# Kernel optimization log

Hardware: AMD Instinct MI355X
Metric: run time of the kernel (lower is better)

The kernel has to match this reference:

```python
import jax, jax.numpy as jnp
import numpy as np
from jax import lax

N, E = 50000, 800000
IN_DIM = 128
HID = 128
HEADS = 8
DPH = HID // HEADS
RH = 128
BETA = 0.1
GAMMA = 1.0
SVI_ITERS = 5
NUM_LAYERS = 2


def seg_lse(z, seg, n):
    # segment-wise logsumexp along axis 0; z: [E] or [E,H]
    m = jax.ops.segment_max(z, seg, num_segments=n)
    m0 = jnp.where(jnp.isfinite(m), m, 0.0)
    s = jax.ops.segment_sum(jnp.exp(z - m0[seg]), seg, num_segments=n)
    return jnp.where(s > 0, jnp.log(jnp.maximum(s, 1e-38)) + m0, -jnp.inf)


def seg_softmax(e, seg, n):
    lse = seg_lse(e, seg, n)
    return jnp.exp(e - lse[seg])


def gat_layer(h_in, W, a_src, a_dst, src, dst, n):
    h = (h_in @ W).reshape(n, HEADS, DPH)                       # [N,H,D]
    al_s = jnp.einsum('nhd,hd->nh', h, a_src)                   # [N,H]
    al_d = jnp.einsum('nhd,hd->nh', h, a_dst)
    e = jax.nn.leaky_relu(al_s[src] + al_d[dst], 0.2)           # [E,H]
    attn = seg_softmax(e, dst, n)                               # softmax over incoming edges
    out = jax.ops.segment_sum(attn[:, :, None] * h[src], dst, num_segments=n)
    return out.reshape(n, HEADS * DPH), attn.mean(-1)           # [N,HID], [E]


def mlp2(z, W1, b1, w2, b2):
    return jax.nn.relu(z @ W1 + b1) @ w2 + b2                   # [E]


def svi_hop(r, src, dst, n, has_out):
    # soft value iteration: V[s] = beta*logsumexp_e(Q_e/beta), Q_e = r_e + gamma*V[dst]
    def body(V, _):
        Q = r + GAMMA * V[dst]
        V2 = jnp.where(has_out, BETA * seg_lse(Q / BETA, src, n), 0.0)
        return V2, None
    V, _ = lax.scan(body, jnp.zeros(n, r.dtype), None, length=SVI_ITERS)
    Q = r + GAMMA * V[dst]
    logz = seg_lse(Q / BETA, src, n)
    log_pi = Q / BETA - logz[src]                               # per-edge log pi*(a|s=src)
    return Q, log_pi


def setup_inputs() -> dict:
    key = jax.random.key(0)
    ks = jax.random.split(key, 20)
    s = 0.05
    inp = {
        'x': jax.random.normal(ks[0], (N, IN_DIM), jnp.float32),
        'edge_index': jax.random.randint(ks[1], (2, E), 0, N, jnp.int64),
        'W0': jax.random.normal(ks[2], (IN_DIM, HID), jnp.float32) * s,
        'as0': jax.random.normal(ks[3], (HEADS, DPH), jnp.float32) * s,
        'ad0': jax.random.normal(ks[4], (HEADS, DPH), jnp.float32) * s,
        'W1': jax.random.normal(ks[5], (HID, HID), jnp.float32) * s,
        'as1': jax.random.normal(ks[6], (HEADS, DPH), jnp.float32) * s,
        'ad1': jax.random.normal(ks[7], (HEADS, DPH), jnp.float32) * s,
        'Ws1': jax.random.normal(ks[8], (4, RH), jnp.float32) * s,
        'bs1': jnp.zeros((RH,), jnp.float32),
        'ws2': jax.random.normal(ks[9], (RH,), jnp.float32) * s,
        'bs2': jnp.zeros((), jnp.float32),
        'Wm1': jax.random.normal(ks[10], (2 * HID, RH), jnp.float32) * s,
        'bm1': jnp.zeros((RH,), jnp.float32),
        'wm2': jax.random.normal(ks[11], (RH,), jnp.float32) * s,
        'bm2': jnp.zeros((), jnp.float32),
        'lam1': jnp.ones((), jnp.float32),
    }
    return inp


def reference(x, edge_index, W0, as0, ad0, W1, as1, ad1,
              Ws1, bs1, ws2, bs2, Wm1, bm1, wm2, bm2, lam1):
    n = x.shape[0]
    src, dst = edge_index[0], edge_index[1]

    # --- GAT encoder trajectory: hidden_per_hop = [x, h1], attn_per_hop = [a1, a2]
    h1, a1 = gat_layer(x, W0, as0, ad0, src, dst, n)
    h1 = jax.nn.elu(h1)
    h2, a2 = gat_layer(h1, W1, as1, ad1, src, dst, n)
    hidden = [x, h1]
    attn = [a1, a2]

    # --- structural per-edge features (degrees)
    ones_e = jnp.ones(src.shape[0], x.dtype)
    deg_out = jax.ops.segment_sum(ones_e, src, num_segments=n)
    deg_in = jax.ops.segment_sum(ones_e, dst, num_segments=n)
    sf = jnp.stack([deg_out[src], deg_in[dst],
                    jnp.log1p(deg_out[src]), jnp.log1p(deg_in[dst])], axis=-1)  # [E,4]
    r_str = mlp2(sf, Ws1, bs1, ws2, bs2)

    has_out = deg_out > 0

    # --- per-hop rewards: r = r_str + lambda1 * r_sem  (use_tmp=False)
    rewards = []
    for t in range(NUM_LAYERS):
        h = hidden[t]
        r_sem = mlp2(jnp.concatenate([h[src], h[dst]], axis=-1), Wm1, bm1, wm2, bm2)
        rewards.append(r_str + lam1 * r_sem)

    # --- soft value iteration per hop
    log_pi_star = [svi_hop(r, src, dst, n, has_out)[1] for r in rewards]

    # --- observed policy from attention (renormalized over outgoing edges)
    log_pi_obs = []
    for a in attn:
        la = jnp.log(a + 1e-12)
        log_pi_obs.append(la - seg_lse(la, src, n)[src])

    # --- NLL loss: sum_t scatter_add(-p_obs * log_pi*) over src, mean over nodes
    per_src_nll = jnp.zeros(n, x.dtype)
    for t in range(NUM_LAYERS):
        p = jnp.exp(log_pi_obs[t])
        per_src_nll = per_src_nll + jax.ops.segment_sum(-p * log_pi_star[t], src, num_segments=n)
    loss = per_src_nll.mean()

    # --- KL(pi_obs || pi*) anomaly score per node
    score = jnp.zeros(n, x.dtype)
    for t in range(NUM_LAYERS):
        p = jnp.exp(log_pi_obs[t])
        score = score + jax.ops.segment_sum(p * (log_pi_obs[t] - log_pi_star[t]), src, num_segments=n)

    return loss, score
```

## Files before the change

kernel.cpp:

```cpp
#include <hip/hip_runtime.h>
#include <math.h>

#define NN 50000
#define NE 800000
#define BETAF 0.1f
#define INVB 10.0f

typedef _Float16 half8v __attribute__((ext_vector_type(8)));
typedef _Float16 half2v __attribute__((ext_vector_type(2)));
typedef float floatx4 __attribute__((ext_vector_type(4)));

__device__ __forceinline__ float sc_(float s, float m, float mn){
  return (s == 0.f) ? 0.f : s * expf(m - mn);
}
__device__ __forceinline__ void red16(float& v){
  v += __shfl_xor(v, 1, 64); v += __shfl_xor(v, 2, 64);
  v += __shfl_xor(v, 4, 64); v += __shfl_xor(v, 8, 64);
}
__device__ __forceinline__ void lse16(float& m, float& s){
  #pragma unroll
  for (int off = 1; off < 16; off <<= 1){
    float mo = __shfl_xor(m, off, 64), so = __shfl_xor(s, off, 64);
    float mn = fmaxf(m, mo);
    s = sc_(s, m, mn) + sc_(so, mo, mn); m = mn;
  }
}
__device__ __forceinline__ float dot2acc(half2v a, half2v b, float c){
#if __has_builtin(__builtin_amdgcn_fdot2)
  return __builtin_amdgcn_fdot2(a, b, c, false);
#else
  return c + (float)a[0]*(float)b[0] + (float)a[1]*(float)b[1];
#endif
}

__launch_bounds__(256)
__global__ void k_hist(const int* __restrict__ ei, int* __restrict__ cs, int* __restrict__ cd){
  int e = blockIdx.x*256 + threadIdx.x;
  if (e >= NE) return;
  atomicAdd(&cs[ei[e]], 1);
  atomicAdd(&cd[ei[NE + e]], 1);
}

__launch_bounds__(256)
__global__ void k_scan_a(const int* __restrict__ inA, const int* __restrict__ inB,
                         int* __restrict__ outA, int* __restrict__ outB,
                         int* __restrict__ partA, int* __restrict__ partB, int n){
  const int* in = blockIdx.y ? inB : inA;
  int* out = blockIdx.y ? outB : outA;
  int* part = blockIdx.y ? partB : partA;
  int i = blockIdx.x*256 + threadIdx.x;
  int v = (i < n) ? in[i] : 0;
  int lane = threadIdx.x & 63, wid = threadIdx.x >> 6;
  int x = v;
  #pragma unroll
  for (int off = 1; off < 64; off <<= 1){
    int t = __shfl_up(x, off, 64);
    if (lane >= off) x += t;
  }
  __shared__ int wsum[4];
  if (lane == 63) wsum[wid] = x;
  __syncthreads();
  int base = 0;
  #pragma unroll
  for (int w = 0; w < 4; ++w) if (w < wid) base += wsum[w];
  if (i < n) out[i] = base + x - v;
  if (threadIdx.x == 255) part[blockIdx.x] = base + x;
}

__launch_bounds__(256)
__global__ void k_scan_b(int* __restrict__ partA, int* __restrict__ partB, int np){
  int* part = blockIdx.y ? partB : partA;
  int i = threadIdx.x;
  int v = (i < np) ? part[i] : 0;
  int lane = threadIdx.x & 63, wid = threadIdx.x >> 6;
  int x = v;
  #pragma unroll
  for (int off = 1; off < 64; off <<= 1){
    int t = __shfl_up(x, off, 64);
    if (lane >= off) x += t;
  }
  __shared__ int wsum[4];
  if (lane == 63) wsum[wid] = x;
  __syncthreads();
  int base = 0;
  #pragma unroll
  for (int w = 0; w < 4; ++w) if (w < wid) base += wsum[w];
  if (i < np) part[i] = base + x - v;
}

__launch_bounds__(256)
__global__ void k_scan_c(int* __restrict__ outA, int* __restrict__ outB,
                         int* __restrict__ curA, int* __restrict__ curB,
                         const int* __restrict__ partA, const int* __restrict__ partB, int n){
  int* out = blockIdx.y ? outB : outA;
  int* cur = blockIdx.y ? curB : curA;
  const int* part = blockIdx.y ? partB : partA;
  int i = blockIdx.x*256 + threadIdx.x;
  if (i < n){
    int f = out[i] + part[blockIdx.x];
    out[i] = f;
    cur[i] = f;
  }
  if (blockIdx.x == 0 && threadIdx.x == 0) out[n] = NE;
}

__launch_bounds__(256)
__global__ void k_scatter(const int* __restrict__ ei, int* __restrict__ cur_s, int* __restrict__ cur_d,
                          int* __restrict__ src_of_j, int* __restrict__ dst_csr,
                          int* __restrict__ src_dord, int* __restrict__ rs_dord){
  int e = blockIdx.x*256 + threadIdx.x;
  if (e >= NE) return;
  int s = ei[e], d = ei[NE + e];
  int js = atomicAdd(&cur_s[s], 1);
  src_of_j[js] = s;
  dst_csr[js] = d;
  int jd = atomicAdd(&cur_d[d], 1);
  src_dord[jd] = s;
  rs_dord[jd] = js;
}

__launch_bounds__(256)
__global__ void k_deg(const int* __restrict__ row_s, const int* __restrict__ row_d,
                      unsigned char* __restrict__ d8o, unsigned char* __restrict__ d8i){
  int n = blockIdx.x*256 + threadIdx.x;
  if (n >= NN) return;
  int a = row_s[n+1] - row_s[n];
  int b = row_d[n+1] - row_d[n];
  d8o[n] = (unsigned char)(a > 127 ? 127 : a);
  d8i[n] = (unsigned char)(b > 127 ? 127 : b);
}

__launch_bounds__(256)
__global__ void k_prepw(const float* __restrict__ W0, const float* __restrict__ W1,
                        const float* __restrict__ Wm1, _Float16* __restrict__ Wt){
  int idx = blockIdx.x*256 + threadIdx.x;
  if (idx >= 4*128*128) return;
  int mat = idx >> 14, rem = idx & 16383;
  int n = rem >> 7, k = rem & 127;
  const float* src = (mat == 0) ? W0 : (mat == 1) ? W1 : (mat == 2) ? Wm1 : (Wm1 + 128*128);
  Wt[idx] = (_Float16)src[k*128 + n];
}

__launch_bounds__(256)
__global__ void k_strtab(const float* __restrict__ Ws1, const float* __restrict__ bs1,
                         const float* __restrict__ ws2, const float* __restrict__ bs2,
                         float* __restrict__ tab){
  int idx = blockIdx.x*256 + threadIdx.x;
  if (idx >= 128*128) return;
  float du = (float)(idx >> 7), di = (float)(idx & 127);
  float lo = log1pf(du), li = log1pf(di);
  float acc = 0.f;
  for (int c = 0; c < 128; ++c){
    float z = du*Ws1[c] + di*Ws1[128+c] + lo*Ws1[256+c] + li*Ws1[384+c] + bs1[c];
    acc += fmaxf(z, 0.f)*ws2[c];
  }
  tab[idx] = acc + bs2[0];
}

template<int AF16, int SECOND>
__launch_bounds__(256)
__global__ void k_gemm3(const void* __restrict__ Ap,
                        const _Float16* __restrict__ Bt0, const _Float16* __restrict__ Bt1,
                        const _Float16* __restrict__ Bt2,
                        const float* __restrict__ bm1,
                        const float* __restrict__ a_s, const float* __restrict__ a_d,
                        _Float16* __restrict__ Hout, _Float16* __restrict__ U01,
                        _Float16* __restrict__ V01,
                        float* __restrict__ alS, float* __restrict__ alD, int M){
  int wv = threadIdx.x >> 6, lane = threadIdx.x & 63;
  int m = lane & 15, q = lane >> 4;
  int row = blockIdx.x*64 + wv*16 + m;
  int arow = (row < M) ? row : (M-1);
  half8v af[4];
  if (AF16){
    const half8v* Ar = (const half8v*)((const _Float16*)Ap + (size_t)arow*128);
    #pragma unroll
    for (int kt = 0; kt < 4; ++kt) af[kt] = Ar[kt*4 + q];
  } else {
    const float* Ar = (const float*)Ap + (size_t)arow*128;
    #pragma unroll
    for (int kt = 0; kt < 4; ++kt){
      const float4* f = (const float4*)(Ar + kt*32 + q*8);
      float4 a0 = f[0], a1 = f[1];
      half8v h;
      h[0]=(_Float16)a0.x; h[1]=(_Float16)a0.y; h[2]=(_Float16)a0.z; h[3]=(_Float16)a0.w;
      h[4]=(_Float16)a1.x; h[5]=(_Float16)a1.y; h[6]=(_Float16)a1.z; h[7]=(_Float16)a1.w;
      af[kt] = h;
    }
  }
  floatx4 acc0[8], acc1[8], acc2[8];
  #pragma unroll
  for (int ct = 0; ct < 8; ++ct){
    #pragma unroll
    for (int r = 0; r < 4; ++r){ acc0[ct][r]=0.f; acc1[ct][r]=0.f; acc2[ct][r]=0.f; }
  }
  #pragma unroll
  for (int ct = 0; ct < 8; ++ct){
    const half8v* Br0 = (const half8v*)(Bt0 + (size_t)(ct*16 + m)*128);
    const half8v* Br1 = (const half8v*)(Bt1 + (size_t)(ct*16 + m)*128);
    const half8v* Br2 = (const half8v*)(Bt2 + (size_t)(ct*16 + m)*128);
    #pragma unroll
    for (int kt = 0; kt < 4; ++kt){
      acc0[ct] = __builtin_amdgcn_mfma_f32_16x16x32_f16(af[kt], Br0[kt*4 + q], acc0[ct], 0, 0, 0);
      acc1[ct] = __builtin_amdgcn_mfma_f32_16x16x32_f16(af[kt], Br1[kt*4 + q], acc1[ct], 0, 0, 0);
      acc2[ct] = __builtin_amdgcn_mfma_f32_16x16x32_f16(af[kt], Br2[kt*4 + q], acc2[ct], 0, 0, 0);
    }
  }
  int rb = blockIdx.x*64 + wv*16 + q*4;
  #pragma unroll
  for (int ct = 0; ct < 8; ++ct){
    float cs = a_s[ct*16 + m], cd = a_d[ct*16 + m];
    #pragma unroll
    for (int r = 0; r < 4; ++r){
      float ps = acc0[ct][r]*cs, pd = acc0[ct][r]*cd;
      #pragma unroll
      for (int off = 1; off < 16; off <<= 1){
        ps += __shfl_xor(ps, off, 64);
        pd += __shfl_xor(pd, off, 64);
      }
      int rr = rb + r;
      if (m == 0 && rr < M){ alS[rr*8 + ct] = ps; alD[rr*8 + ct] = pd; }
    }
  }
  #pragma unroll
  for (int ct = 0; ct < 8; ++ct){
    int col = ct*16 + m;
    float bv = bm1[col];
    #pragma unroll
    for (int r = 0; r < 4; ++r){
      int rr = rb + r;
      if (rr < M){
        if (SECOND == 0) Hout[(size_t)rr*128 + col] = (_Float16)acc0[ct][r];
        U01[(size_t)rr*256 + SECOND*128 + col] = (_Float16)(acc1[ct][r] + bv);
        V01[(size_t)rr*256 + SECOND*128 + col] = (_Float16)acc2[ct][r];
      }
    }
  }
}

template<bool AGG>
__launch_bounds__(256)
__global__ void k_att(const int* __restrict__ row_d, const int* __restrict__ src_dord,
                      const int* __restrict__ rs_dord,
                      const float* __restrict__ alS, const float* __restrict__ alD,
                      const _Float16* __restrict__ H,
                      float* __restrict__ a_csr, _Float16* __restrict__ h1){
  __shared__ float zbuf[4][64*8];
  int wv = threadIdx.x >> 6;
  int node = blockIdx.x*4 + wv;
  if (node >= NN) return;
  int lane = threadIdx.x & 63;
  int j0 = row_d[node], j1 = row_d[node+1];
  int deg = j1 - j0;
  if (deg == 0){
    if (AGG){
      half2v z; z[0] = (_Float16)0; z[1] = (_Float16)0;
      ((half2v*)(h1 + (size_t)node*128))[lane] = z;
    }
    return;
  }
  int head = lane & 7, slot = lane >> 3;
  float ad = alD[node*8 + head];
  float m = -INFINITY, ssum = 0.f;

  if (deg <= 64){
    for (int e = slot; e < deg; e += 8){
      int s = src_dord[j0 + e];
      float z = alS[s*8 + head] + ad;
      z = (z >= 0.f) ? z : 0.2f*z;
      zbuf[wv][e*8 + head] = z;
      float mn = fmaxf(m, z);
      ssum = sc_(ssum, m, mn) + expf(z - mn);
      m = mn;
    }
    #pragma unroll
    for (int off = 8; off < 64; off <<= 1){
      float mo = __shfl_xor(m, off, 64);
      float so = __shfl_xor(ssum, off, 64);
      float mn = fmaxf(m, mo);
      ssum = sc_(ssum, m, mn) + sc_(so, mo, mn);
      m = mn;
    }
    float inv_s = 1.f / ssum;
    for (int e = slot; e < deg; e += 8){
      float a = expf(zbuf[wv][e*8 + head] - m) * inv_s;
      zbuf[wv][e*8 + head] = a;
      float asum = a;
      asum += __shfl_xor(asum, 1, 64);
      asum += __shfl_xor(asum, 2, 64);
      asum += __shfl_xor(asum, 4, 64);
      if (head == 0) a_csr[rs_dord[j0 + e]] = asum * 0.125f;
    }
    if (AGG){
      __asm__ volatile("s_waitcnt lgkmcnt(0)" ::: "memory");
      int h2 = lane >> 3;
      float ax = 0.f, ay = 0.f;
      const half2v* Hv = (const half2v*)H;
      for (int e = 0; e < deg; ++e){
        int s = src_dord[j0 + e];
        float a = zbuf[wv][e*8 + h2];
        half2v hv = Hv[(size_t)s*64 + lane];
        ax += a*(float)hv[0];
        ay += a*(float)hv[1];
      }
      ax = (ax > 0.f) ? ax : expm1f(ax);
      ay = (ay > 0.f) ? ay : expm1f(ay);
      half2v o; o[0] = (_Float16)ax; o[1] = (_Float16)ay;
      ((half2v*)(h1 + (size_t)node*128))[lane] = o;
    }
  } else {
    for (int j = j0 + slot; j < j1; j += 8){
      int s = src_dord[j];
      float z = alS[s*8 + head] + ad;
      z = (z >= 0.f) ? z : 0.2f*z;
      float mn = fmaxf(m, z);
      ssum = sc_(ssum, m, mn) + expf(z - mn);
      m = mn;
    }
    #pragma unroll
    for (int off = 8; off < 64; off <<= 1){
      float mo = __shfl_xor(m, off, 64);
      float so = __shfl_xor(ssum, off, 64);
      float mn = fmaxf(m, mo);
      ssum = sc_(ssum, m, mn) + sc_(so, mo, mn);
      m = mn;
    }
    float inv_s = 1.f / ssum;
    for (int j = j0 + slot; j < j1; j += 8){
      int s = src_dord[j];
      float z = alS[s*8 + head] + ad;
      z = (z >= 0.f) ? z : 0.2f*z;
      float a = expf(z - m) * inv_s;
      float asum = a;
      asum += __shfl_xor(asum, 1, 64);
      asum += __shfl_xor(asum, 2, 64);
      asum += __shfl_xor(asum, 4, 64);
      if (head == 0) a_csr[rs_dord[j]] = asum * 0.125f;
    }
    if (AGG){
      int h2 = lane >> 3;
      float m2 = __shfl(m, h2*8, 64);
      float is2 = __shfl(inv_s, h2*8, 64);
      float ad2 = alD[node*8 + h2];
      float ax = 0.f, ay = 0.f;
      const half2v* Hv = (const half2v*)H;
      for (int j = j0; j < j1; ++j){
        int s = src_dord[j];
        float z = alS[s*8 + h2] + ad2;
        z = (z >= 0.f) ? z : 0.2f*z;
        float a = expf(z - m2) * is2;
        half2v hv = Hv[(size_t)s*64 + lane];
        ax += a*(float)hv[0];
        ay += a*(float)hv[1];
      }
      ax = (ax > 0.f) ? ax : expm1f(ax);
      ay = (ay > 0.f) ? ay : expm1f(ay);
      half2v o; o[0] = (_Float16)ax; o[1] = (_Float16)ay;
      ((half2v*)(h1 + (size_t)node*128))[lane] = o;
    }
  }
}

__launch_bounds__(256)
__global__ void k_edge5(const int* __restrict__ src_of_j, const int* __restrict__ dst_csr,
                        const unsigned char* __restrict__ d8o, const unsigned char* __restrict__ d8i,
                        const float* __restrict__ tab,
                        const _Float16* __restrict__ U01, const _Float16* __restrict__ V01,
                        const float* __restrict__ wm2, const float* __restrict__ bm2,
                        const float* __restrict__ lam1,
                        float* __restrict__ rcsr0, float* __restrict__ rcsr1){
  __shared__ _Float16 wml[128];
  if (threadIdx.x < 128) wml[threadIdx.x] = (_Float16)wm2[threadIdx.x];
  __syncthreads();
  int j = blockIdx.x*16 + (threadIdx.x >> 4);
  if (j >= NE) return;
  int t = threadIdx.x & 15;
  int s = src_of_j[j], d = dst_csr[j];
  const half8v* ur = (const half8v*)(U01 + (size_t)s*256);
  const half8v* vr = (const half8v*)(V01 + (size_t)d*256);
  half8v a = ur[t] + vr[t];
  half8v b = ur[16 + t] + vr[16 + t];
  #pragma unroll
  for (int k = 0; k < 8; ++k){
    a[k] = (a[k] > (_Float16)0) ? a[k] : (_Float16)0;
    b[k] = (b[k] > (_Float16)0) ? b[k] : (_Float16)0;
  }
  const half8v* wl = (const half8v*)wml;
  half8v w = wl[t];
  float r0 = 0.f, r1 = 0.f;
  #pragma unroll
  for (int c = 0; c < 4; ++c){
    half2v aa = {a[2*c], a[2*c+1]};
    half2v bb = {b[2*c], b[2*c+1]};
    half2v ww = {w[2*c], w[2*c+1]};
    r0 = dot2acc(aa, ww, r0);
    r1 = dot2acc(bb, ww, r1);
  }
  red16(r0); red16(r1);
  if (t == 0){
    float rstr = tab[((int)d8o[s] << 7) | (int)d8i[d]];
    float lam = lam1[0], bb2 = bm2[0];
    rcsr0[j] = rstr + lam*(r0 + bb2);
    rcsr1[j] = rstr + lam*(r1 + bb2);
  }
}

__launch_bounds__(256)
__global__ void k_svi(const int* __restrict__ row_s, const int* __restrict__ dst_csr,
                      const float* __restrict__ r0, const float* __restrict__ r1,
                      const float* __restrict__ V0in, const float* __restrict__ V1in,
                      float* __restrict__ out0, float* __restrict__ out1){
  int node = blockIdx.x*16 + (threadIdx.x >> 4);
  if (node >= NN) return;
  int t = threadIdx.x & 15;
  int j0 = row_s[node], j1 = row_s[node+1];
  if (j0 == j1){
    if (t == 0){ out0[node] = 0.f; out1[node] = 0.f; }
    return;
  }
  float m0 = -INFINITY, s0 = 0.f, m1 = -INFINITY, s1 = 0.f;
  for (int j = j0 + t; j < j1; j += 16){
    int d = dst_csr[j];
    float q0 = (r0[j] + V0in[d]) * INVB;
    float q1 = (r1[j] + V1in[d]) * INVB;
    float mn0 = fmaxf(m0, q0);
    s0 = sc_(s0, m0, mn0) + expf(q0 - mn0); m0 = mn0;
    float mn1 = fmaxf(m1, q1);
    s1 = sc_(s1, m1, mn1) + expf(q1 - mn1); m1 = mn1;
  }
  lse16(m0, s0); lse16(m1, s1);
  if (t == 0){
    out0[node] = BETAF*(logf(s0) + m0);
    out1[node] = BETAF*(logf(s1) + m1);
  }
}

__launch_bounds__(256)
__global__ void k_final2(const int* __restrict__ row_s, const int* __restrict__ dst_csr,
                         const float* __restrict__ a0, const float* __restrict__ a1,
                         const float* __restrict__ r0, const float* __restrict__ r1,
                         const float* __restrict__ V0, const float* __restrict__ V1,
                         float* __restrict__ out, float* __restrict__ partial){
  int node = blockIdx.x*16 + (threadIdx.x >> 4);
  int t = threadIdx.x & 15;
  float nll = 0.f;
  if (node < NN){
    int j0 = row_s[node], j1 = row_s[node+1];
    if (j0 == j1){
      if (t == 0) out[1 + node] = 0.f;
    } else {
      float mq0=-INFINITY, sq0=0.f, mq1=-INFINITY, sq1=0.f;
      float ma0=-INFINITY, sa0=0.f, ma1=-INFINITY, sa1=0.f;
      for (int j = j0 + t; j < j1; j += 16){
        int d = dst_csr[j];
        float q0 = (r0[j] + V0[d]) * INVB;
        float q1 = (r1[j] + V1[d]) * INVB;
        float la0 = logf(a0[j] + 1e-12f);
        float la1 = logf(a1[j] + 1e-12f);
        float mn;
        mn = fmaxf(mq0, q0); sq0 = sc_(sq0, mq0, mn) + expf(q0 - mn); mq0 = mn;
        mn = fmaxf(mq1, q1); sq1 = sc_(sq1, mq1, mn) + expf(q1 - mn); mq1 = mn;
        mn = fmaxf(ma0, la0); sa0 = sc_(sa0, ma0, mn) + expf(la0 - mn); ma0 = mn;
        mn = fmaxf(ma1, la1); sa1 = sc_(sa1, ma1, mn) + expf(la1 - mn); ma1 = mn;
      }
      lse16(mq0, sq0); lse16(mq1, sq1); lse16(ma0, sa0); lse16(ma1, sa1);
      float L0 = logf(sq0) + mq0, L1 = logf(sq1) + mq1;
      float O0 = logf(sa0) + ma0, O1 = logf(sa1) + ma1;
      float sca = 0.f;
      for (int j = j0 + t; j < j1; j += 16){
        int d = dst_csr[j];
        float la0 = logf(a0[j] + 1e-12f);
        float lp0 = la0 - O0;
        float p0 = expf(lp0);
        float ls0 = (r0[j] + V0[d]) * INVB - L0;
        nll -= p0 * ls0;
        sca += p0 * (lp0 - ls0);
        float la1 = logf(a1[j] + 1e-12f);
        float lp1 = la1 - O1;
        float p1 = expf(lp1);
        float ls1 = (r1[j] + V1[d]) * INVB - L1;
        nll -= p1 * ls1;
        sca += p1 * (lp1 - ls1);
      }
      red16(sca);
      if (t == 0) out[1 + node] = sca;
    }
  }
  #pragma unroll
  for (int off = 1; off < 64; off <<= 1) nll += __shfl_xor(nll, off, 64);
  __shared__ float wsum[4];
  if ((threadIdx.x & 63) == 0) wsum[threadIdx.x >> 6] = nll;
  __syncthreads();
  if (threadIdx.x == 0) partial[blockIdx.x] = wsum[0]+wsum[1]+wsum[2]+wsum[3];
}

__launch_bounds__(256)
__global__ void k_nllred(const float* __restrict__ partial, int np, float* __restrict__ out){
  float s = 0.f;
  for (int i = threadIdx.x; i < np; i += 256) s += partial[i];
  #pragma unroll
  for (int off = 1; off < 64; off <<= 1) s += __shfl_xor(s, off, 64);
  __shared__ float wsum[4];
  if ((threadIdx.x & 63) == 0) wsum[threadIdx.x >> 6] = s;
  __syncthreads();
  if (threadIdx.x == 0) out[0] = (wsum[0]+wsum[1]+wsum[2]+wsum[3]) * (1.f/NN);
}

extern "C" void kernel_launch(void* const* d_in, const int* in_sizes, int n_in,
                              void* d_out, int out_size, void* d_ws, size_t ws_size,
                              hipStream_t stream){
  const float* x    = (const float*)d_in[0];
  const int*   ei   = (const int*)d_in[1];
  const float* W0   = (const float*)d_in[2];
  const float* as0  = (const float*)d_in[3];
  const float* ad0  = (const float*)d_in[4];
  const float* W1   = (const float*)d_in[5];
  const float* as1  = (const float*)d_in[6];
  const float* ad1  = (const float*)d_in[7];
  const float* Ws1  = (const float*)d_in[8];
  const float* bs1  = (const float*)d_in[9];
  const float* ws2  = (const float*)d_in[10];
  const float* bs2  = (const float*)d_in[11];
  const float* Wm1  = (const float*)d_in[12];
  const float* bm1  = (const float*)d_in[13];
  const float* wm2  = (const float*)d_in[14];
  const float* bm2  = (const float*)d_in[15];
  const float* lam1 = (const float*)d_in[16];
  float* out = (float*)d_out;

  char* p = (char*)d_ws;
  auto alloc = [&](size_t bytes)->void*{
    void* r = (void*)p;
    p += (bytes + 255) & ~(size_t)255;
    return r;
  };
  _Float16* Hh   = (_Float16*)alloc((size_t)NN*128*2);
  _Float16* h1f  = (_Float16*)alloc((size_t)NN*128*2);
  _Float16* U01  = (_Float16*)alloc((size_t)NN*256*2);
  _Float16* V01  = (_Float16*)alloc((size_t)NN*256*2);
  _Float16* Wt   = (_Float16*)alloc((size_t)4*128*128*2);
  float* tab     = (float*)alloc((size_t)128*128*4);
  int*   src_of_j= (int*)alloc((size_t)NE*4);
  int*   dst_csr = (int*)alloc((size_t)NE*4);
  int*   src_dord= (int*)alloc((size_t)NE*4);
  int*   rs_dord = (int*)alloc((size_t)NE*4);
  int*   row_s   = (int*)alloc((size_t)(NN+1)*4);
  int*   row_d   = (int*)alloc((size_t)(NN+1)*4);
  int*   cur_s   = (int*)alloc((size_t)NN*4);
  int*   cur_d   = (int*)alloc((size_t)NN*4);
  int*   partA   = (int*)alloc(256*4);
  int*   partB   = (int*)alloc(256*4);
  unsigned char* d8o = (unsigned char*)alloc(NN);
  unsigned char* d8i = (unsigned char*)alloc(NN);
  float* alS     = (float*)alloc((size_t)NN*8*4);
  float* alD     = (float*)alloc((size_t)NN*8*4);
  float* acsr0   = (float*)alloc((size_t)NE*4);
  float* acsr1   = (float*)alloc((size_t)NE*4);
  float* rcsr0   = (float*)alloc((size_t)NE*4);
  float* rcsr1   = (float*)alloc((size_t)NE*4);
  float* V0a = (float*)alloc((size_t)NN*4);
  float* V0b = (float*)alloc((size_t)NN*4);
  float* V1a = (float*)alloc((size_t)NN*4);
  float* V1b = (float*)alloc((size_t)NN*4);
  float* nllpart = (float*)alloc((size_t)4*((NN+15)/16 + 1));

  _Float16* W0t = Wt;
  _Float16* W1t = Wt + 128*128;
  _Float16* Wut = Wt + 2*128*128;
  _Float16* Wvt = Wt + 3*128*128;

  const int G_E    = (NE + 255)/256;
  const int G_gemm = (NN + 63)/64;
  const int G_n4   = (NN + 3)/4;
  const int G_n16  = (NN + 15)/16;
  const int G_e16  = (NE + 15)/16;
  const int NPART  = (NN + 255)/256;

  hipMemsetAsync(cur_s, 0, (size_t)NN*4, stream);
  hipMemsetAsync(cur_d, 0, (size_t)NN*4, stream);
  k_hist<<<G_E, 256, 0, stream>>>(ei, cur_s, cur_d);
  k_scan_a<<<dim3(NPART,2), 256, 0, stream>>>(cur_s, cur_d, row_s, row_d, partA, partB, NN);
  k_scan_b<<<dim3(1,2), 256, 0, stream>>>(partA, partB, NPART);
  k_scan_c<<<dim3(NPART,2), 256, 0, stream>>>(row_s, row_d, cur_s, cur_d, partA, partB, NN);
  k_scatter<<<G_E, 256, 0, stream>>>(ei, cur_s, cur_d, src_of_j, dst_csr, src_dord, rs_dord);
  k_deg<<<(NN+255)/256, 256, 0, stream>>>(row_s, row_d, d8o, d8i);

  k_prepw<<<(4*128*128+255)/256, 256, 0, stream>>>(W0, W1, Wm1, Wt);
  k_strtab<<<(128*128+255)/256, 256, 0, stream>>>(Ws1, bs1, ws2, bs2, tab);

  k_gemm3<0,0><<<G_gemm, 256, 0, stream>>>(x, W0t, Wut, Wvt, bm1, as0, ad0,
                                           Hh, U01, V01, alS, alD, NN);
  k_att<true><<<G_n4, 256, 0, stream>>>(row_d, src_dord, rs_dord, alS, alD, Hh, acsr0, h1f);

  k_gemm3<1,1><<<G_gemm, 256, 0, stream>>>(h1f, W1t, Wut, Wvt, bm1, as1, ad1,
                                           nullptr, U01, V01, alS, alD, NN);
  k_att<false><<<G_n4, 256, 0, stream>>>(row_d, src_dord, rs_dord, alS, alD, nullptr, acsr1, nullptr);

  k_edge5<<<G_e16, 256, 0, stream>>>(src_of_j, dst_csr, d8o, d8i, tab,
                                     U01, V01, wm2, bm2, lam1, rcsr0, rcsr1);

  hipMemsetAsync(V0a, 0, (size_t)NN*4, stream);
  hipMemsetAsync(V1a, 0, (size_t)NN*4, stream);
  float* v0i = V0a; float* v0o = V0b;
  float* v1i = V1a; float* v1o = V1b;
  for (int it = 0; it < 5; ++it){
    k_svi<<<G_n16, 256, 0, stream>>>(row_s, dst_csr, rcsr0, rcsr1, v0i, v1i, v0o, v1o);
    float* t;
    t = v0i; v0i = v0o; v0o = t;
    t = v1i; v1i = v1o; v1o = t;
  }

  k_final2<<<G_n16, 256, 0, stream>>>(row_s, dst_csr, acsr0, acsr1, rcsr0, rcsr1,
                                      v0i, v1i, out, nllpart);
  k_nllred<<<1, 256, 0, stream>>>(nllpart, G_n16, out);
}
```

Measured before the change: 710.0 us.

## Pack edge index arrays, fuse SVI iterations cooperatively, precompute log attention

```diff
diff --git a/kernel.cpp b/kernel.cpp
--- a/kernel.cpp
+++ b/kernel.cpp
@@ -1,10 +1,11 @@
 #include <hip/hip_runtime.h>
+#include <hip/hip_cooperative_groups.h>
 #include <math.h>
+
+namespace cg = cooperative_groups;
 
 #define NN 50000
 #define NE 800000
-#define BETAF 0.1f
-#define INVB 10.0f
 
 typedef _Float16 half8v __attribute__((ext_vector_type(8)));
 typedef _Float16 half2v __attribute__((ext_vector_type(2)));
@@ -106,17 +107,14 @@
 
 __launch_bounds__(256)
 __global__ void k_scatter(const int* __restrict__ ei, int* __restrict__ cur_s, int* __restrict__ cur_d,
-                          int* __restrict__ src_of_j, int* __restrict__ dst_csr,
-                          int* __restrict__ src_dord, int* __restrict__ rs_dord){
+                          int2* __restrict__ sd_csr, int2* __restrict__ sr_dord){
   int e = blockIdx.x*256 + threadIdx.x;
   if (e >= NE) return;
   int s = ei[e], d = ei[NE + e];
   int js = atomicAdd(&cur_s[s], 1);
-  src_of_j[js] = s;
-  dst_csr[js] = d;
+  sd_csr[js] = make_int2(s, d);
   int jd = atomicAdd(&cur_d[d], 1);
-  src_dord[jd] = s;
-  rs_dord[jd] = js;
+  sr_dord[jd] = make_int2(s, js);
 }
 
 __launch_bounds__(256)
@@ -240,11 +238,10 @@
 
 template<bool AGG>
 __launch_bounds__(256)
-__global__ void k_att(const int* __restrict__ row_d, const int* __restrict__ src_dord,
-                      const int* __restrict__ rs_dord,
+__global__ void k_att(const int* __restrict__ row_d, const int2* __restrict__ sr_dord,
                       const float* __restrict__ alS, const float* __restrict__ alD,
                       const _Float16* __restrict__ H,
-                      float* __restrict__ a_csr, _Float16* __restrict__ h1){
+                      float* __restrict__ la_csr, _Float16* __restrict__ h1){
   __shared__ float zbuf[4][64*8];
   int wv = threadIdx.x >> 6;
   int node = blockIdx.x*4 + wv;
@@ -265,7 +262,7 @@
 
   if (deg <= 64){
     for (int e = slot; e < deg; e += 8){
-      int s = src_dord[j0 + e];
+      int s = sr_dord[j0 + e].x;
       float z = alS[s*8 + head] + ad;
       z = (z >= 0.f) ? z : 0.2f*z;
       zbuf[wv][e*8 + head] = z;
@@ -289,7 +286,7 @@
       asum += __shfl_xor(asum, 1, 64);
       asum += __shfl_xor(asum, 2, 64);
       asum += __shfl_xor(asum, 4, 64);
-      if (head == 0) a_csr[rs_dord[j0 + e]] = asum * 0.125f;
+      if (head == 0) la_csr[sr_dord[j0 + e].y] = logf(asum*0.125f + 1e-12f);
     }
     if (AGG){
       __asm__ volatile("s_waitcnt lgkmcnt(0)" ::: "memory");
@@ -297,7 +294,7 @@
       float ax = 0.f, ay = 0.f;
       const half2v* Hv = (const half2v*)H;
       for (int e = 0; e < deg; ++e){
-        int s = src_dord[j0 + e];
+        int s = sr_dord[j0 + e].x;
         float a = zbuf[wv][e*8 + h2];
         half2v hv = Hv[(size_t)s*64 + lane];
         ax += a*(float)hv[0];
@@ -310,7 +307,7 @@
     }
   } else {
     for (int j = j0 + slot; j < j1; j += 8){
-      int s = src_dord[j];
+      int s = sr_dord[j].x;
       float z = alS[s*8 + head] + ad;
       z = (z >= 0.f) ? z : 0.2f*z;
       float mn = fmaxf(m, z);
@@ -327,7 +324,7 @@
     }
     float inv_s = 1.f / ssum;
     for (int j = j0 + slot; j < j1; j += 8){
-      int s = src_dord[j];
+      int s = sr_dord[j].x;
       float z = alS[s*8 + head] + ad;
       z = (z >= 0.f) ? z : 0.2f*z;
       float a = expf(z - m) * inv_s;
@@ -335,7 +332,7 @@
       asum += __shfl_xor(asum, 1, 64);
       asum += __shfl_xor(asum, 2, 64);
       asum += __shfl_xor(asum, 4, 64);
-      if (head == 0) a_csr[rs_dord[j]] = asum * 0.125f;
+      if (head == 0) la_csr[sr_dord[j].y] = logf(asum*0.125f + 1e-12f);
     }
     if (AGG){
       int h2 = lane >> 3;
@@ -345,7 +342,7 @@
       float ax = 0.f, ay = 0.f;
       const half2v* Hv = (const half2v*)H;
       for (int j = j0; j < j1; ++j){
-        int s = src_dord[j];
+        int s = sr_dord[j].x;
         float z = alS[s*8 + h2] + ad2;
         z = (z >= 0.f) ? z : 0.2f*z;
         float a = expf(z - m2) * is2;
@@ -362,7 +359,7 @@
 }
 
 __launch_bounds__(256)
-__global__ void k_edge5(const int* __restrict__ src_of_j, const int* __restrict__ dst_csr,
+__global__ void k_edge5(const int2* __restrict__ sd,
                         const unsigned char* __restrict__ d8o, const unsigned char* __restrict__ d8i,
                         const float* __restrict__ tab,
                         const _Float16* __restrict__ U01, const _Float16* __restrict__ V01,
@@ -375,7 +372,8 @@
   int j = blockIdx.x*16 + (threadIdx.x >> 4);
   if (j >= NE) return;
   int t = threadIdx.x & 15;
-  int s = src_of_j[j], d = dst_csr[j];
+  int2 sdv = sd[j];
+  int s = sdv.x, d = sdv.y;
   const half8v* ur = (const half8v*)(U01 + (size_t)s*256);
   const half8v* vr = (const half8v*)(V01 + (size_t)d*256);
   half8v a = ur[t] + vr[t];
@@ -400,44 +398,54 @@
   if (t == 0){
     float rstr = tab[((int)d8o[s] << 7) | (int)d8i[d]];
     float lam = lam1[0], bb2 = bm2[0];
-    rcsr0[j] = rstr + lam*(r0 + bb2);
-    rcsr1[j] = rstr + lam*(r1 + bb2);
-  }
-}
-
-__launch_bounds__(256)
-__global__ void k_svi(const int* __restrict__ row_s, const int* __restrict__ dst_csr,
-                      const float* __restrict__ r0, const float* __restrict__ r1,
-                      const float* __restrict__ V0in, const float* __restrict__ V1in,
-                      float* __restrict__ out0, float* __restrict__ out1){
-  int node = blockIdx.x*16 + (threadIdx.x >> 4);
-  if (node >= NN) return;
+    rcsr0[j] = 10.f*(rstr + lam*(r0 + bb2));
+    rcsr1[j] = 10.f*(rstr + lam*(r1 + bb2));
+  }
+}
+
+__launch_bounds__(256)
+__global__ void k_svi5(const int* __restrict__ row_s, const int2* __restrict__ sd,
+                       const float* __restrict__ r0, const float* __restrict__ r1,
+                       float* __restrict__ VA0, float* __restrict__ VB0,
+                       float* __restrict__ VA1, float* __restrict__ VB1){
+  cg::grid_group grid = cg::this_grid();
   int t = threadIdx.x & 15;
-  int j0 = row_s[node], j1 = row_s[node+1];
-  if (j0 == j1){
-    if (t == 0){ out0[node] = 0.f; out1[node] = 0.f; }
-    return;
-  }
-  float m0 = -INFINITY, s0 = 0.f, m1 = -INFINITY, s1 = 0.f;
-  for (int j = j0 + t; j < j1; j += 16){
-    int d = dst_csr[j];
-    float q0 = (r0[j] + V0in[d]) * INVB;
-    float q1 = (r1[j] + V1in[d]) * INVB;
-    float mn0 = fmaxf(m0, q0);
-    s0 = sc_(s0, m0, mn0) + expf(q0 - mn0); m0 = mn0;
-    float mn1 = fmaxf(m1, q1);
-    s1 = sc_(s1, m1, mn1) + expf(q1 - mn1); m1 = mn1;
-  }
-  lse16(m0, s0); lse16(m1, s1);
-  if (t == 0){
-    out0[node] = BETAF*(logf(s0) + m0);
-    out1[node] = BETAF*(logf(s1) + m1);
-  }
-}
-
-__launch_bounds__(256)
-__global__ void k_final2(const int* __restrict__ row_s, const int* __restrict__ dst_csr,
-                         const float* __restrict__ a0, const float* __restrict__ a1,
+  int g0 = blockIdx.x*16 + (threadIdx.x >> 4);
+  int stride = gridDim.x*16;
+  for (int it = 0; it < 5; ++it){
+    const float* v0i = (it & 1) ? VB0 : VA0;
+    float* v0o = (it & 1) ? VA0 : VB0;
+    const float* v1i = (it & 1) ? VB1 : VA1;
+    float* v1o = (it & 1) ? VA1 : VB1;
+    for (int node = g0; node < NN; node += stride){
+      int j0 = row_s[node], j1 = row_s[node+1];
+      if (j0 == j1){
+        if (t == 0){ v0o[node] = 0.f; v1o[node] = 0.f; }
+        continue;
+      }
+      float m0 = -INFINITY, s0 = 0.f, m1 = -INFINITY, s1 = 0.f;
+      for (int j = j0 + t; j < j1; j += 16){
+        int d = sd[j].y;
+        float q0 = r0[j] + v0i[d];
+        float q1 = r1[j] + v1i[d];
+        float mn0 = fmaxf(m0, q0);
+        s0 = sc_(s0, m0, mn0) + expf(q0 - mn0); m0 = mn0;
+        float mn1 = fmaxf(m1, q1);
+        s1 = sc_(s1, m1, mn1) + expf(q1 - mn1); m1 = mn1;
+      }
+      lse16(m0, s0); lse16(m1, s1);
+      if (t == 0){
+        v0o[node] = logf(s0) + m0;
+        v1o[node] = logf(s1) + m1;
+      }
+    }
+    grid.sync();
+  }
+}
+
+__launch_bounds__(256)
+__global__ void k_final2(const int* __restrict__ row_s, const int2* __restrict__ sd,
+                         const float* __restrict__ la0, const float* __restrict__ la1,
                          const float* __restrict__ r0, const float* __restrict__ r1,
                          const float* __restrict__ V0, const float* __restrict__ V1,
                          float* __restrict__ out, float* __restrict__ partial){
@@ -446,39 +454,78 @@
   float nll = 0.f;
   if (node < NN){
     int j0 = row_s[node], j1 = row_s[node+1];
-    if (j0 == j1){
+    int deg = j1 - j0;
+    if (deg == 0){
       if (t == 0) out[1 + node] = 0.f;
+    } else if (deg <= 32){
+      int ja = j0 + t, jb = j0 + t + 16;
+      float q0a=-INFINITY,q1a=-INFINITY,l0a=-INFINITY,l1a=-INFINITY;
+      float q0b=-INFINITY,q1b=-INFINITY,l0b=-INFINITY,l1b=-INFINITY;
+      if (ja < j1){
+        int d = sd[ja].y;
+        q0a = r0[ja] + V0[d]; q1a = r1[ja] + V1[d];
+        l0a = la0[ja]; l1a = la1[ja];
+      }
+      if (jb < j1){
+        int d = sd[jb].y;
+        q0b = r0[jb] + V0[d]; q1b = r1[jb] + V1[d];
+        l0b = la0[jb]; l1b = la1[jb];
+      }
+      float mq0 = fmaxf(q0a, q0b), mq1 = fmaxf(q1a, q1b);
+      float ml0 = fmaxf(l0a, l0b), ml1 = fmaxf(l1a, l1b);
+      float sq0 = 0.f, sq1 = 0.f, sl0 = 0.f, sl1 = 0.f;
+      if (q0a != -INFINITY) sq0 += expf(q0a - mq0);
+      if (q0b != -INFINITY) sq0 += expf(q0b - mq0);
+      if (q1a != -INFINITY) sq1 += expf(q1a - mq1);
+      if (q1b != -INFINITY) sq1 += expf(q1b - mq1);
+      if (l0a != -INFINITY) sl0 += expf(l0a - ml0);
+      if (l0b != -INFINITY) sl0 += expf(l0b - ml0);
+      if (l1a != -INFINITY) sl1 += expf(l1a - ml1);
+      if (l1b != -INFINITY) sl1 += expf(l1b - ml1);
+      lse16(mq0, sq0); lse16(mq1, sq1); lse16(ml0, sl0); lse16(ml1, sl1);
+      float L0 = logf(sq0) + mq0, L1 = logf(sq1) + mq1;
+      float O0 = logf(sl0) + ml0, O1 = logf(sl1) + ml1;
+      float sca = 0.f;
+      if (ja < j1){
+        float lp0 = l0a - O0, p0 = expf(lp0), ls0 = q0a - L0;
+        nll -= p0*ls0; sca += p0*(lp0 - ls0);
+        float lp1 = l1a - O1, p1 = expf(lp1), ls1 = q1a - L1;
+        nll -= p1*ls1; sca += p1*(lp1 - ls1);
+      }
+      if (jb < j1){
+        float lp0 = l0b - O0, p0 = expf(lp0), ls0 = q0b - L0;
+        nll -= p0*ls0; sca += p0*(lp0 - ls0);
+        float lp1 = l1b - O1, p1 = expf(lp1), ls1 = q1b - L1;
+        nll -= p1*ls1; sca += p1*(lp1 - ls1);
+      }
+      red16(sca);
+      if (t == 0) out[1 + node] = sca;
     } else {
       float mq0=-INFINITY, sq0=0.f, mq1=-INFINITY, sq1=0.f;
       float ma0=-INFINITY, sa0=0.f, ma1=-INFINITY, sa1=0.f;
       for (int j = j0 + t; j < j1; j += 16){
-        int d = dst_csr[j];
-        float q0 = (r0[j] + V0[d]) * INVB;
-        float q1 = (r1[j] + V1[d]) * INVB;
-        float la0 = logf(a0[j] + 1e-12f);
-        float la1 = logf(a1[j] + 1e-12f);
+        int d = sd[j].y;
+        float q0 = r0[j] + V0[d];
+        float q1 = r1[j] + V1[d];
+        float v0 = la0[j], v1 = la1[j];
         float mn;
         mn = fmaxf(mq0, q0); sq0 = sc_(sq0, mq0, mn) + expf(q0 - mn); mq0 = mn;
         mn = fmaxf(mq1, q1); sq1 = sc_(sq1, mq1, mn) + expf(q1 - mn); mq1 = mn;
-        mn = fmaxf(ma0, la0); sa0 = sc_(sa0, ma0, mn) + expf(la0 - mn); ma0 = mn;
-        mn = fmaxf(ma1, la1); sa1 = sc_(sa1, ma1, mn) + expf(la1 - mn); ma1 = mn;
+        mn = fmaxf(ma0, v0); sa0 = sc_(sa0, ma0, mn) + expf(v0 - mn); ma0 = mn;
+        mn = fmaxf(ma1, v1); sa1 = sc_(sa1, ma1, mn) + expf(v1 - mn); ma1 = mn;
       }
       lse16(mq0, sq0); lse16(mq1, sq1); lse16(ma0, sa0); lse16(ma1, sa1);
       float L0 = logf(sq0) + mq0, L1 = logf(sq1) + mq1;
       float O0 = logf(sa0) + ma0, O1 = logf(sa1) + ma1;
       float sca = 0.f;
       for (int j = j0 + t; j < j1; j += 16){
-        int d = dst_csr[j];
-        float la0 = logf(a0[j] + 1e-12f);
-        float lp0 = la0 - O0;
-        float p0 = expf(lp0);
-        float ls0 = (r0[j] + V0[d]) * INVB - L0;
+        int d = sd[j].y;
+        float lp0 = la0[j] - O0, p0 = expf(lp0);
+        float ls0 = (r0[j] + V0[d]) - L0;
         nll -= p0 * ls0;
         sca += p0 * (lp0 - ls0);
-        float la1 = logf(a1[j] + 1e-12f);
-        float lp1 = la1 - O1;
-        float p1 = expf(lp1);
-        float ls1 = (r1[j] + V1[d]) * INVB - L1;
+        float lp1 = la1[j] - O1, p1 = expf(lp1);
+        float ls1 = (r1[j] + V1[d]) - L1;
         nll -= p1 * ls1;
         sca += p1 * (lp1 - ls1);
       }
@@ -540,10 +587,8 @@
   _Float16* V01  = (_Float16*)alloc((size_t)NN*256*2);
   _Float16* Wt   = (_Float16*)alloc((size_t)4*128*128*2);
   float* tab     = (float*)alloc((size_t)128*128*4);
-  int*   src_of_j= (int*)alloc((size_t)NE*4);
-  int*   dst_csr = (int*)alloc((size_t)NE*4);
-  int*   src_dord= (int*)alloc((size_t)NE*4);
-  int*   rs_dord = (int*)alloc((size_t)NE*4);
+  int2*  sd_csr  = (int2*)alloc((size_t)NE*8);
+  int2*  sr_dord = (int2*)alloc((size_t)NE*8);
   int*   row_s   = (int*)alloc((size_t)(NN+1)*4);
   int*   row_d   = (int*)alloc((size_t)(NN+1)*4);
   int*   cur_s   = (int*)alloc((size_t)NN*4);
@@ -582,7 +627,7 @@
   k_scan_a<<<dim3(NPART,2), 256, 0, stream>>>(cur_s, cur_d, row_s, row_d, partA, partB, NN);
   k_scan_b<<<dim3(1,2), 256, 0, stream>>>(partA, partB, NPART);
   k_scan_c<<<dim3(NPART,2), 256, 0, stream>>>(row_s, row_d, cur_s, cur_d, partA, partB, NN);
-  k_scatter<<<G_E, 256, 0, stream>>>(ei, cur_s, cur_d, src_of_j, dst_csr, src_dord, rs_dord);
+  k_scatter<<<G_E, 256, 0, stream>>>(ei, cur_s, cur_d, sd_csr, sr_dord);
   k_deg<<<(NN+255)/256, 256, 0, stream>>>(row_s, row_d, d8o, d8i);
 
   k_prepw<<<(4*128*128+255)/256, 256, 0, stream>>>(W0, W1, Wm1, Wt);
@@ -590,27 +635,24 @@
 
   k_gemm3<0,0><<<G_gemm, 256, 0, stream>>>(x, W0t, Wut, Wvt, bm1, as0, ad0,
                                            Hh, U01, V01, alS, alD, NN);
-  k_att<true><<<G_n4, 256, 0, stream>>>(row_d, src_dord, rs_dord, alS, alD, Hh, acsr0, h1f);
+  k_att<true><<<G_n4, 256, 0, stream>>>(row_d, sr_dord, alS, alD, Hh, acsr0, h1f);
 
   k_gemm3<1,1><<<G_gemm, 256, 0, stream>>>(h1f, W1t, Wut, Wvt, bm1, as1, ad1,
                                            nullptr, U01, V01, alS, alD, NN);
-  k_att<false><<<G_n4, 256, 0, stream>>>(row_d, src_dord, rs_dord, alS, alD, nullptr, acsr1, nullptr);
-
-  k_edge5<<<G_e16, 256, 0, stream>>>(src_of_j, dst_csr, d8o, d8i, tab,
+  k_att<false><<<G_n4, 256, 0, stream>>>(row_d, sr_dord, alS, alD, nullptr, acsr1, nullptr);
+
+  k_edge5<<<G_e16, 256, 0, stream>>>(sd_csr, d8o, d8i, tab,
                                      U01, V01, wm2, bm2, lam1, rcsr0, rcsr1);
 
   hipMemsetAsync(V0a, 0, (size_t)NN*4, stream);
   hipMemsetAsync(V1a, 0, (size_t)NN*4, stream);
-  float* v0i = V0a; float* v0o = V0b;
-  float* v1i = V1a; float* v1o = V1b;
-  for (int it = 0; it < 5; ++it){
-    k_svi<<<G_n16, 256, 0, stream>>>(row_s, dst_csr, rcsr0, rcsr1, v0i, v1i, v0o, v1o);
-    float* t;
-    t = v0i; v0i = v0o; v0o = t;
-    t = v1i; v1i = v1o; v1o = t;
-  }
-
-  k_final2<<<G_n16, 256, 0, stream>>>(row_s, dst_csr, acsr0, acsr1, rcsr0, rcsr1,
-                                      v0i, v1i, out, nllpart);
+  {
+    void* args[] = {(void*)&row_s, (void*)&sd_csr, (void*)&rcsr0, (void*)&rcsr1,
+                    (void*)&V0a, (void*)&V0b, (void*)&V1a, (void*)&V1b};
+    hipLaunchCooperativeKernel((const void*)k_svi5, dim3(1024), dim3(256), args, 0, stream);
+  }
+
+  k_final2<<<G_n16, 256, 0, stream>>>(row_s, sd_csr, acsr0, acsr1, rcsr0, rcsr1,
+                                      V0b, V1b, out, nllpart);
   k_nllred<<<1, 256, 0, stream>>>(nllpart, G_n16, out);
 }
```

Result: slower. 1.438 ms (+102.5%).
